# Kernel tuning notes

Measured on AMD Instinct MI355X. Metric: run time of the kernel, lower is better.

## Reference

```python
import jax, jax.numpy as jnp
import numpy as np

EPS = 1e-5  # BatchNorm eps

def _bn(x):
    # BatchNorm1d(affine=False) in training mode: per-agent, per-feature batch stats
    m = jnp.mean(x, axis=1, keepdims=True)
    v = jnp.var(x, axis=1, keepdims=True)
    return (x - m) / jnp.sqrt(v + EPS)

def _lrelu(x):
    return jax.nn.leaky_relu(x, 0.01)

def setup_inputs() -> dict:
    key = jax.random.key(0)
    ks = jax.random.split(key, 14)
    A, B, IN, OUT, H, K = 8, 32768, 128, 32, 128, 4
    D = H // K
    s = 0.05
    return {
        "states": jax.random.normal(ks[0], (A, B, IN), jnp.float32),
        "actions": jax.random.normal(ks[1], (A, B, OUT), jnp.float32),
        "enc_w": jax.random.normal(ks[2], (A, IN + OUT, H), jnp.float32) * s,
        "enc_b": jax.random.normal(ks[3], (A, H), jnp.float32) * s,
        "aenc_w": jax.random.normal(ks[4], (A, OUT, H), jnp.float32) * s,
        "aenc_b": jax.random.normal(ks[5], (A, H), jnp.float32) * s,
        "key_w": jax.random.normal(ks[6], (K, H, D), jnp.float32) * s,
        "sel_w": jax.random.normal(ks[7], (K, H, D), jnp.float32) * s,
        "val_w": jax.random.normal(ks[8], (K, H, D), jnp.float32) * s,
        "val_b": jax.random.normal(ks[9], (K, D), jnp.float32) * s,
        "c1_w": jax.random.normal(ks[10], (A, 2 * H, H), jnp.float32) * s,
        "c1_b": jax.random.normal(ks[11], (A, H), jnp.float32) * s,
        "c2_w": jax.random.normal(ks[12], (A, H, 1), jnp.float32) * s,
        "c2_b": jax.random.normal(ks[13], (A, 1), jnp.float32) * s,
    }

def reference(states, actions, enc_w, enc_b, aenc_w, aenc_b,
              key_w, sel_w, val_w, val_b, c1_w, c1_b, c2_w, c2_b):
    A, B, _ = states.shape
    # per-agent state-action encodings: [A,B,H]
    sa = _bn(jnp.concatenate([states, actions], axis=-1))
    sa_enc = _lrelu(jnp.einsum('abi,aih->abh', sa, enc_w) + enc_b[:, None, :])
    # per-agent action encodings: [A,B,H]
    a_in = _bn(actions)
    a_enc = _lrelu(jnp.einsum('abi,aih->abh', a_in, aenc_w) + aenc_b[:, None, :])
    # per-head keys/values/selectors: [K,A,B,D]
    keys = jnp.einsum('abh,khd->kabd', a_enc, key_w)
    vals = _lrelu(jnp.einsum('abh,khd->kabd', a_enc, val_w) + val_b[:, None, None, :])
    sels = jnp.einsum('abh,khd->kabd', sa_enc, sel_w)
    D = keys.shape[-1]
    # attention logits over other agents: [K,B,A_query,A_key], self excluded
    logits = jnp.einsum('kibd,kjbd->kbij', sels, keys) / jnp.sqrt(jnp.float32(D))
    self_mask = jnp.eye(A, dtype=bool)[None, None]
    probs = jax.nn.softmax(jnp.where(self_mask, -jnp.inf, logits), axis=-1)
    # attended values: [K,A,B,D] -> concat heads -> [A,B,K*D]
    other = jnp.einsum('kbij,kjbd->kibd', probs, vals)
    other_cat = jnp.transpose(other, (1, 2, 0, 3)).reshape(A, B, -1)
    # per-agent critics on [sa_enc, attended]: [A,B,1]
    critic_in = jnp.concatenate([sa_enc, other_cat], axis=-1)
    h = _lrelu(jnp.einsum('abi,aih->abh', critic_in, c1_w) + c1_b[:, None, :])
    q = jnp.einsum('abh,aho->abo', h, c2_w) + c2_b[:, None, :]
    return q
```

## Files before the change

kernel.cpp:

```cpp
#include <hip/hip_runtime.h>
#include <hip/hip_bf16.h>
#include <stdint.h>

#define A_N 8
#define B_N 32768
#define IN_N 128
#define OUT_N 32
#define SAF 160
#define H_N 128
#define D_N 32
#define KD_N 128
#define CIN_N 256
#define CHUNKS 128
#define EPSV 1e-5f
#define ENC_KP 192

typedef unsigned int u32;
typedef unsigned short u16;
typedef __attribute__((ext_vector_type(8))) short short8;
typedef __attribute__((ext_vector_type(4))) float floatx4;

__device__ __forceinline__ float bf_lo(u32 u){ return __uint_as_float(u << 16); }
__device__ __forceinline__ float bf_hi(u32 u){ return __uint_as_float(u & 0xffff0000u); }
__device__ __forceinline__ float bf2f(u16 b){ return __uint_as_float(((u32)b) << 16); }
__device__ __forceinline__ u16 f2bf(float f){
  u32 u = __float_as_uint(f);
  return (u16)((u + 0x7fffu + ((u >> 16) & 1u)) >> 16);
}
__device__ __forceinline__ float lrelu(float x){ return x > 0.f ? x : 0.01f * x; }

__global__ __launch_bounds__(256) void k_stats(
    const float* __restrict__ states, const float* __restrict__ actions,
    float* __restrict__ part)
{
  int a = blockIdx.y;
  int chunk = blockIdx.x;
  int t = threadIdx.x;
  int r0 = chunk * (B_N / CHUNKS);
  __shared__ float red[512];
  {
    int f = t & 127, half = t >> 7;
    const float* p = states + ((size_t)a * B_N + r0 + half) * IN_N + f;
    float s1 = 0.f, s2 = 0.f;
    for (int it = 0; it < 128; ++it){
      float v = p[(size_t)(2 * it) * IN_N];
      s1 += v; s2 += v * v;
    }
    red[t] = s1; red[256 + t] = s2;
    __syncthreads();
    if (t < 128){
      float a1 = red[t] + red[t + 128];
      float a2 = red[256 + t] + red[256 + t + 128];
      size_t o = (((size_t)a * CHUNKS + chunk) * SAF + t) * 2;
      part[o] = a1; part[o + 1] = a2;
    }
    __syncthreads();
  }
  {
    int f = t & 31, g = t >> 5;
    const float* p = actions + ((size_t)a * B_N + r0 + g) * OUT_N + f;
    float s1 = 0.f, s2 = 0.f;
    for (int it = 0; it < 32; ++it){
      float v = p[(size_t)(8 * it) * OUT_N];
      s1 += v; s2 += v * v;
    }
    red[t] = s1; red[256 + t] = s2;
    __syncthreads();
    if (t < 32){
      float a1 = 0.f, a2 = 0.f;
      #pragma unroll
      for (int gg = 0; gg < 8; ++gg){
        a1 += red[t + 32 * gg];
        a2 += red[256 + t + 32 * gg];
      }
      size_t o = (((size_t)a * CHUNKS + chunk) * SAF + 128 + t) * 2;
      part[o] = a1; part[o + 1] = a2;
    }
  }
}

__global__ void k_finalize(const float* __restrict__ part,
                           float* __restrict__ meanArr, float* __restrict__ istdArr)
{
  int idx = blockIdx.x * blockDim.x + threadIdx.x;
  if (idx >= A_N * SAF) return;
  int a = idx / SAF, f = idx % SAF;
  float s1 = 0.f, s2 = 0.f;
  for (int c = 0; c < CHUNKS; ++c){
    size_t o = (((size_t)a * CHUNKS + c) * SAF + f) * 2;
    s1 += part[o]; s2 += part[o + 1];
  }
  float m = s1 * (1.f / B_N);
  float v = s2 * (1.f / B_N) - m * m;
  if (v < 0.f) v = 0.f;
  meanArr[idx] = m;
  istdArr[idx] = rsqrtf(v + EPSV);
}

__device__ __forceinline__ void packpair(float w, u16* __restrict__ dh,
                                         u16* __restrict__ dl, int i){
  u16 h = f2bf(w);
  dh[i] = h;
  dl[i] = f2bf(w - bf2f(h));
}

__global__ __launch_bounds__(256) void k_pack(
    const float* __restrict__ enc_w, const float* __restrict__ aenc_w,
    const float* __restrict__ key_w, const float* __restrict__ sel_w,
    const float* __restrict__ val_w, const float* __restrict__ c1_w,
    u16* __restrict__ encH, u16* __restrict__ encL,
    u16* __restrict__ aencH, u16* __restrict__ aencL,
    u16* __restrict__ keyH, u16* __restrict__ selH, u16* __restrict__ valH,
    u16* __restrict__ c1H, u16* __restrict__ c1L)
{
  int i = blockIdx.x * 256 + threadIdx.x;
  const int S0 = A_N * H_N * ENC_KP;
  const int S1 = A_N * H_N * OUT_N;
  const int S2 = KD_N * H_N;
  const int S5 = A_N * H_N * CIN_N;
  if (i < S0){
    int a = i / (H_N * ENC_KP); int r = i % (H_N * ENC_KP);
    int n = r / ENC_KP; int k = r % ENC_KP;
    float v = (k < SAF) ? enc_w[((size_t)a * SAF + k) * H_N + n] : 0.f;
    packpair(v, encH, encL, i);
    return;
  }
  i -= S0;
  if (i < S1){
    int a = i / (H_N * OUT_N); int r = i % (H_N * OUT_N);
    int n = r / OUT_N; int k = r % OUT_N;
    packpair(aenc_w[((size_t)a * OUT_N + k) * H_N + n], aencH, aencL, i);
    return;
  }
  i -= S1;
  if (i < 3 * S2){
    int which = i / S2; int j = i % S2;
    int n = j / H_N, k = j % H_N;
    const float* w = (which == 0) ? key_w : ((which == 1) ? sel_w : val_w);
    u16* dh = (which == 0) ? keyH : ((which == 1) ? selH : valH);
    dh[j] = f2bf(w[(((size_t)(n >> 5)) * H_N + k) * D_N + (n & 31)]);
    return;
  }
  i -= 3 * S2;
  if (i < S5){
    int a = i / (H_N * CIN_N); int r = i % (H_N * CIN_N);
    int n = r / CIN_N; int k = r % CIN_N;
    packpair(c1_w[((size_t)a * CIN_N + k) * H_N + n], c1H, c1L, i);
  }
}
#define PACK_TOTAL (A_N*H_N*ENC_KP + A_N*H_N*OUT_N + 3*KD_N*H_N + A_N*H_N*CIN_N)

__global__ __launch_bounds__(256, 3) void k_enc_sel(
    const float* __restrict__ states, const float* __restrict__ actions,
    const float* __restrict__ mean, const float* __restrict__ istd,
    const u16* __restrict__ encH, const u16* __restrict__ encL,
    const float* __restrict__ enc_b,
    const u16* __restrict__ selH,
    u16* __restrict__ sa_enc, u16* __restrict__ sels)
{
  int a = blockIdx.y; int row0 = blockIdx.x * 128; int t = threadIdx.x;
  int lane = t & 63, wave = t >> 6, l16 = lane & 15, quad = lane >> 4;
  __shared__ __align__(16) u16 S[22528];
  __shared__ __align__(16) float sc[192], sh[192];
  u16* Wh = S;
  u16* Wl = S + 5120;
  u16* Xh = S + 10240;
  u16* Xl = S + 15360;
  u16* T  = S;
  u16* Ws = S + 17408;

  if (t < 192){
    float m = 0.f, s = 0.f;
    if (t < SAF){ m = mean[a * SAF + t]; s = istd[a * SAF + t]; }
    sc[t] = s; sh[t] = -m * s;
  }
  floatx4 acc[2][8];
  #pragma unroll
  for (int mt = 0; mt < 2; ++mt)
    #pragma unroll
    for (int nt = 0; nt < 8; ++nt) acc[mt][nt] = (floatx4){0.f,0.f,0.f,0.f};
  const u16* wbh = encH + (size_t)a * H_N * ENC_KP;
  const u16* wbl = encL + (size_t)a * H_N * ENC_KP;
  __syncthreads();

  for (int k0 = 0; k0 < ENC_KP; k0 += 32){
    for (int c = t; c < 512; c += 256){
      int n = c >> 2, off = (c & 3) * 8;
      *(uint4*)&Wh[n * 40 + off] = *(const uint4*)(wbh + (size_t)n * ENC_KP + k0 + off);
      *(uint4*)&Wl[n * 40 + off] = *(const uint4*)(wbl + (size_t)n * ENC_KP + k0 + off);
    }
    for (int c = t; c < 1024; c += 256){
      int r = c >> 3, kc = (c & 7) * 4, f = k0 + kc;
      size_t row = (size_t)a * B_N + row0 + r;
      float4 v = {0.f, 0.f, 0.f, 0.f};
      if (f < IN_N)     v = *(const float4*)(states + row * IN_N + f);
      else if (f < SAF) v = *(const float4*)(actions + row * OUT_N + (f - IN_N));
      float4 scv = *(const float4*)&sc[f];
      float4 shv = *(const float4*)&sh[f];
      float x0 = fmaf(v.x, scv.x, shv.x), x1 = fmaf(v.y, scv.y, shv.y);
      float x2 = fmaf(v.z, scv.z, shv.z), x3 = fmaf(v.w, scv.w, shv.w);
      u16 h0 = f2bf(x0), h1 = f2bf(x1), h2 = f2bf(x2), h3 = f2bf(x3);
      *(u32*)&Xh[r * 40 + kc]     = (u32)h0 | ((u32)h1 << 16);
      *(u32*)&Xh[r * 40 + kc + 2] = (u32)h2 | ((u32)h3 << 16);
      u16 l0 = f2bf(x0 - bf2f(h0)), l1 = f2bf(x1 - bf2f(h1));
      u16 l2 = f2bf(x2 - bf2f(h2)), l3 = f2bf(x3 - bf2f(h3));
      *(u32*)&Xl[r * 40 + kc]     = (u32)l0 | ((u32)l1 << 16);
      *(u32*)&Xl[r * 40 + kc + 2] = (u32)l2 | ((u32)l3 << 16);
    }
    __syncthreads();
    {
      short8 ah[2], al[2], bh[8], bl[8];
      #pragma unroll
      for (int mt = 0; mt < 2; ++mt){
        int rr = (wave * 32 + mt * 16 + l16) * 40 + quad * 8;
        ah[mt] = *(const short8*)&Xh[rr];
        al[mt] = *(const short8*)&Xl[rr];
      }
      #pragma unroll
      for (int nt = 0; nt < 8; ++nt){
        int rr = (nt * 16 + l16) * 40 + quad * 8;
        bh[nt] = *(const short8*)&Wh[rr];
        bl[nt] = *(const short8*)&Wl[rr];
      }
      #pragma unroll
      for (int mt = 0; mt < 2; ++mt)
        #pragma unroll
        for (int nt = 0; nt < 8; ++nt){
          acc[mt][nt] = __builtin_amdgcn_mfma_f32_16x16x32_bf16(ah[mt], bh[nt], acc[mt][nt], 0,0,0);
          acc[mt][nt] = __builtin_amdgcn_mfma_f32_16x16x32_bf16(ah[mt], bl[nt], acc[mt][nt], 0,0,0);
          acc[mt][nt] = __builtin_amdgcn_mfma_f32_16x16x32_bf16(al[mt], bh[nt], acc[mt][nt], 0,0,0);
        }
    }
    __syncthreads();
  }

  {
    float bv[8];
    #pragma unroll
    for (int nt = 0; nt < 8; ++nt) bv[nt] = enc_b[a * H_N + nt * 16 + l16];
    #pragma unroll
    for (int mt = 0; mt < 2; ++mt)
      #pragma unroll
      for (int nt = 0; nt < 8; ++nt)
        #pragma unroll
        for (int r = 0; r < 4; ++r){
          int rl = wave * 32 + mt * 16 + quad * 4 + r;
          T[rl * 136 + nt * 16 + l16] = f2bf(lrelu(acc[mt][nt][r] + bv[nt]));
        }
  }
  __syncthreads();
  for (int c = t; c < 2048; c += 256){
    int row = c >> 4, col8 = (c & 15) * 8;
    *(uint4*)(sa_enc + ((size_t)a * B_N + row0 + row) * H_N + col8) =
        *(const uint4*)&T[row * 136 + col8];
  }

  #pragma unroll
  for (int mt = 0; mt < 2; ++mt)
    #pragma unroll
    for (int nt = 0; nt < 8; ++nt) acc[mt][nt] = (floatx4){0.f,0.f,0.f,0.f};
  for (int k0 = 0; k0 < H_N; k0 += 32){
    for (int c = t; c < 512; c += 256){
      int n = c >> 2, off = (c & 3) * 8;
      *(uint4*)&Ws[n * 40 + off] = *(const uint4*)(selH + (size_t)n * H_N + k0 + off);
    }
    __syncthreads();
    {
      short8 ah[2], bh[8];
      #pragma unroll
      for (int mt = 0; mt < 2; ++mt)
        ah[mt] = *(const short8*)&T[(wave * 32 + mt * 16 + l16) * 136 + k0 + quad * 8];
      #pragma unroll
      for (int nt = 0; nt < 8; ++nt)
        bh[nt] = *(const short8*)&Ws[(nt * 16 + l16) * 40 + quad * 8];
      #pragma unroll
      for (int mt = 0; mt < 2; ++mt)
        #pragma unroll
        for (int nt = 0; nt < 8; ++nt)
          acc[mt][nt] = __builtin_amdgcn_mfma_f32_16x16x32_bf16(ah[mt], bh[nt], acc[mt][nt], 0,0,0);
    }
    __syncthreads();
  }
  #pragma unroll
  for (int mt = 0; mt < 2; ++mt)
    #pragma unroll
    for (int nt = 0; nt < 8; ++nt)
      #pragma unroll
      for (int r = 0; r < 4; ++r){
        int rl = wave * 32 + mt * 16 + quad * 4 + r;
        T[rl * 136 + nt * 16 + l16] = f2bf(acc[mt][nt][r]);
      }
  __syncthreads();
  for (int c = t; c < 2048; c += 256){
    int row = c >> 4, col8 = (c & 15) * 8;
    *(uint4*)(sels + ((size_t)a * B_N + row0 + row) * H_N + col8) =
        *(const uint4*)&T[row * 136 + col8];
  }
}

__global__ __launch_bounds__(256, 2) void k_aenc_kv(
    const float* __restrict__ actions,
    const float* __restrict__ mean, const float* __restrict__ istd,
    const u16* __restrict__ aencH, const u16* __restrict__ aencL,
    const float* __restrict__ aenc_b,
    const u16* __restrict__ keyH, const u16* __restrict__ valH,
    const float* __restrict__ val_b,
    u16* __restrict__ keys, u16* __restrict__ vals)
{
  int a = blockIdx.y; int row0 = blockIdx.x * 128; int t = threadIdx.x;
  int lane = t & 63, wave = t >> 6, l16 = lane & 15, quad = lane >> 4;
  __shared__ __align__(16) u16 S[35840];
  __shared__ __align__(16) float sc[32], sh[32];
  u16* T  = S;
  u16* WK = S + 17408;
  u16* WV = S + 26624;
  u16* T2 = S + 17408;

  if (t < 32){
    float m = mean[a * SAF + 128 + t], s = istd[a * SAF + 128 + t];
    sc[t] = s; sh[t] = -m * s;
  }
  floatx4 accK[2][8], accV[2][8];
  #pragma unroll
  for (int mt = 0; mt < 2; ++mt)
    #pragma unroll
    for (int nt = 0; nt < 8; ++nt){
      accK[mt][nt] = (floatx4){0.f,0.f,0.f,0.f};
      accV[mt][nt] = (floatx4){0.f,0.f,0.f,0.f};
    }
  __syncthreads();

  {
    u16* Wh1 = S;  u16* Wl1 = S + 5120;
    u16* Xh = S + 10240; u16* Xl = S + 15360;
    const u16* wbh = aencH + (size_t)a * H_N * OUT_N;
    const u16* wbl = aencL + (size_t)a * H_N * OUT_N;
    for (int c = t; c < 512; c += 256){
      int n = c >> 2, off = (c & 3) * 8;
      *(uint4*)&Wh1[n * 40 + off] = *(const uint4*)(wbh + (size_t)n * OUT_N + off);
      *(uint4*)&Wl1[n * 40 + off] = *(const uint4*)(wbl + (size_t)n * OUT_N + off);
    }
    for (int c = t; c < 1024; c += 256){
      int r = c >> 3, kc = (c & 7) * 4;
      size_t row = (size_t)a * B_N + row0 + r;
      float4 v = *(const float4*)(actions + row * OUT_N + kc);
      float4 scv = *(const float4*)&sc[kc];
      float4 shv = *(const float4*)&sh[kc];
      float x0 = fmaf(v.x, scv.x, shv.x), x1 = fmaf(v.y, scv.y, shv.y);
      float x2 = fmaf(v.z, scv.z, shv.z), x3 = fmaf(v.w, scv.w, shv.w);
      u16 h0 = f2bf(x0), h1 = f2bf(x1), h2 = f2bf(x2), h3 = f2bf(x3);
      *(u32*)&Xh[r * 40 + kc]     = (u32)h0 | ((u32)h1 << 16);
      *(u32*)&Xh[r * 40 + kc + 2] = (u32)h2 | ((u32)h3 << 16);
      u16 l0 = f2bf(x0 - bf2f(h0)), l1 = f2bf(x1 - bf2f(h1));
      u16 l2 = f2bf(x2 - bf2f(h2)), l3 = f2bf(x3 - bf2f(h3));
      *(u32*)&Xl[r * 40 + kc]     = (u32)l0 | ((u32)l1 << 16);
      *(u32*)&Xl[r * 40 + kc + 2] = (u32)l2 | ((u32)l3 << 16);
    }
    __syncthreads();
    short8 ah[2], al[2], bh[8], bl[8];
    #pragma unroll
    for (int mt = 0; mt < 2; ++mt){
      int rr = (wave * 32 + mt * 16 + l16) * 40 + quad * 8;
      ah[mt] = *(const short8*)&Xh[rr];
      al[mt] = *(const short8*)&Xl[rr];
    }
    #pragma unroll
    for (int nt = 0; nt < 8; ++nt){
      int rr = (nt * 16 + l16) * 40 + quad * 8;
      bh[nt] = *(const short8*)&Wh1[rr];
      bl[nt] = *(const short8*)&Wl1[rr];
    }
    #pragma unroll
    for (int mt = 0; mt < 2; ++mt)
      #pragma unroll
      for (int nt = 0; nt < 8; ++nt){
        accK[mt][nt] = __builtin_amdgcn_mfma_f32_16x16x32_bf16(ah[mt], bh[nt], accK[mt][nt], 0,0,0);
        accK[mt][nt] = __builtin_amdgcn_mfma_f32_16x16x32_bf16(ah[mt], bl[nt], accK[mt][nt], 0,0,0);
        accK[mt][nt] = __builtin_amdgcn_mfma_f32_16x16x32_bf16(al[mt], bh[nt], accK[mt][nt], 0,0,0);
      }
    __syncthreads();
  }
  {
    float bv[8];
    #pragma unroll
    for (int nt = 0; nt < 8; ++nt) bv[nt] = aenc_b[a * H_N + nt * 16 + l16];
    #pragma unroll
    for (int mt = 0; mt < 2; ++mt)
      #pragma unroll
      for (int nt = 0; nt < 8; ++nt){
        #pragma unroll
        for (int r = 0; r < 4; ++r){
          int rl = wave * 32 + mt * 16 + quad * 4 + r;
          T[rl * 136 + nt * 16 + l16] = f2bf(lrelu(accK[mt][nt][r] + bv[nt]));
        }
        accK[mt][nt] = (floatx4){0.f,0.f,0.f,0.f};
      }
  }

  for (int k0 = 0; k0 < H_N; k0 += 64){
    __syncthreads();
    for (int c = t; c < 1024; c += 256){
      int n = c >> 3, off = (c & 7) * 8;
      *(uint4*)&WK[n * 72 + off] = *(const uint4*)(keyH + (size_t)n * H_N + k0 + off);
      *(uint4*)&WV[n * 72 + off] = *(const uint4*)(valH + (size_t)n * H_N + k0 + off);
    }
    __syncthreads();
    #pragma unroll
    for (int ks = 0; ks < 64; ks += 32){
      short8 ah[2], bk[8], bv[8];
      #pragma unroll
      for (int mt = 0; mt < 2; ++mt)
        ah[mt] = *(const short8*)&T[(wave * 32 + mt * 16 + l16) * 136 + k0 + ks + quad * 8];
      #pragma unroll
      for (int nt = 0; nt < 8; ++nt){
        int rr = (nt * 16 + l16) * 72 + ks + quad * 8;
        bk[nt] = *(const short8*)&WK[rr];
        bv[nt] = *(const short8*)&WV[rr];
      }
      #pragma unroll
      for (int mt = 0; mt < 2; ++mt)
        #pragma unroll
        for (int nt = 0; nt < 8; ++nt){
          accK[mt][nt] = __builtin_amdgcn_mfma_f32_16x16x32_bf16(ah[mt], bk[nt], accK[mt][nt], 0,0,0);
          accV[mt][nt] = __builtin_amdgcn_mfma_f32_16x16x32_bf16(ah[mt], bv[nt], accV[mt][nt], 0,0,0);
        }
    }
  }
  __syncthreads();
  {
    float bv[8];
    #pragma unroll
    for (int nt = 0; nt < 8; ++nt) bv[nt] = val_b[nt * 16 + l16];
    #pragma unroll
    for (int mt = 0; mt < 2; ++mt)
      #pragma unroll
      for (int nt = 0; nt < 8; ++nt)
        #pragma unroll
        for (int r = 0; r < 4; ++r){
          int rl = wave * 32 + mt * 16 + quad * 4 + r;
          T[rl * 136 + nt * 16 + l16]  = f2bf(lrelu(accV[mt][nt][r] + bv[nt]));
          T2[rl * 136 + nt * 16 + l16] = f2bf(accK[mt][nt][r]);
        }
  }
  __syncthreads();
  for (int c = t; c < 2048; c += 256){
    int row = c >> 4, col8 = (c & 15) * 8;
    *(uint4*)(vals + ((size_t)a * B_N + row0 + row) * H_N + col8) =
        *(const uint4*)&T[row * 136 + col8];
    *(uint4*)(keys + ((size_t)a * B_N + row0 + row) * H_N + col8) =
        *(const uint4*)&T2[row * 136 + col8];
  }
}

__global__ __launch_bounds__(256) void k_attn(
    const u16* __restrict__ sels, const u16* __restrict__ keys,
    const u16* __restrict__ vals, u16* __restrict__ other)
{
  int b0 = blockIdx.x * 8;
  int t = threadIdx.x;
  __shared__ __align__(16) u16 sS[8192], sK[8192], sV[8192];
  u32* dS = (u32*)sS; u32* dK = (u32*)sK; u32* dV = (u32*)sV;
  #pragma unroll
  for (int a = 0; a < 8; ++a){
    size_t go = ((size_t)a * B_N + b0) * KD_N;
    const u32* gs = (const u32*)(sels + go);
    const u32* gk = (const u32*)(keys + go);
    const u32* gv = (const u32*)(vals + go);
    dS[a * 512 + t] = gs[t]; dS[a * 512 + 256 + t] = gs[256 + t];
    dK[a * 512 + t] = gk[t]; dK[a * 512 + 256 + t] = gk[256 + t];
    dV[a * 512 + t] = gv[t]; dV[a * 512 + 256 + t] = gv[256 + t];
  }
  __syncthreads();
  int i = t & 7, p = t >> 3;
  int k = p & 3, bl = p >> 2;
  int base_i = (i * 8 + bl) * 128 + k * 32;
  float si[32];
  {
    const u32* S32 = (const u32*)&sS[base_i];
    #pragma unroll
    for (int d2 = 0; d2 < 16; ++d2){
      u32 u = S32[d2];
      si[2 * d2] = bf_lo(u); si[2 * d2 + 1] = bf_hi(u);
    }
  }
  float lg[8];
  #pragma unroll
  for (int j = 0; j < 8; ++j){
    const u32* K32 = (const u32*)&sK[(j * 8 + bl) * 128 + k * 32];
    float acc = 0.f;
    #pragma unroll
    for (int d2 = 0; d2 < 16; ++d2){
      u32 u = K32[d2];
      acc = fmaf(si[2 * d2], bf_lo(u), acc);
      acc = fmaf(si[2 * d2 + 1], bf_hi(u), acc);
    }
    lg[j] = acc * 0.17677669529663689f;
  }
  float mx = -3.0e38f;
  #pragma unroll
  for (int j = 0; j < 8; ++j) if (j != i) mx = fmaxf(mx, lg[j]);
  float pe[8], se = 0.f;
  #pragma unroll
  for (int j = 0; j < 8; ++j){
    pe[j] = (j == i) ? 0.f : __expf(lg[j] - mx);
    se += pe[j];
  }
  float inv = 1.f / se;
  #pragma unroll
  for (int j = 0; j < 8; ++j) pe[j] *= inv;
  __align__(16) u16 ob[32];
  #pragma unroll
  for (int d2 = 0; d2 < 16; ++d2){
    float acc0 = 0.f, acc1 = 0.f;
    #pragma unroll
    for (int j = 0; j < 8; ++j){
      u32 u = *(const u32*)&sV[(j * 8 + bl) * 128 + k * 32 + 2 * d2];
      acc0 = fmaf(pe[j], bf_lo(u), acc0);
      acc1 = fmaf(pe[j], bf_hi(u), acc1);
    }
    ob[2 * d2] = f2bf(acc0); ob[2 * d2 + 1] = f2bf(acc1);
  }
  uint4* dst = (uint4*)(other + ((size_t)i * B_N + (b0 + bl)) * KD_N + k * 32);
  const uint4* s4 = (const uint4*)ob;
  #pragma unroll
  for (int c = 0; c < 4; ++c) dst[c] = s4[c];
}

__global__ __launch_bounds__(256, 3) void k_critic(
    const u16* __restrict__ sa_enc, const u16* __restrict__ other,
    const u16* __restrict__ c1H, const u16* __restrict__ c1L,
    const float* __restrict__ c1_b,
    const float* __restrict__ c2w, const float* __restrict__ c2b,
    float* __restrict__ qout)
{
  int a = blockIdx.y; int row0 = blockIdx.x * 128; int t = threadIdx.x;
  int lane = t & 63, wave = t >> 6, l16 = lane & 15, quad = lane >> 4;
  __shared__ __align__(16) u16 Xs[5120];
  __shared__ __align__(16) u16 Wh[5120];
  __shared__ __align__(16) u16 Wl[5120];
  floatx4 acc[2][8];
  #pragma unroll
  for (int mt = 0; mt < 2; ++mt)
    #pragma unroll
    for (int nt = 0; nt < 8; ++nt) acc[mt][nt] = (floatx4){0.f,0.f,0.f,0.f};
  const u16* wbh = c1H + (size_t)a * H_N * CIN_N;
  const u16* wbl = c1L + (size_t)a * H_N * CIN_N;

  for (int k0 = 0; k0 < CIN_N; k0 += 32){
    for (int c = t; c < 512; c += 256){
      int n = c >> 2, off = (c & 3) * 8;
      *(uint4*)&Wh[n * 40 + off] = *(const uint4*)(wbh + (size_t)n * CIN_N + k0 + off);
      *(uint4*)&Wl[n * 40 + off] = *(const uint4*)(wbl + (size_t)n * CIN_N + k0 + off);
    }
    for (int c = t; c < 512; c += 256){
      int r = c >> 2, off = (c & 3) * 8;
      int fo = k0 + off;
      const u16* src = sa_enc;
      if (fo >= H_N){ src = other; fo -= H_N; }
      *(uint4*)&Xs[r * 40 + off] =
          *(const uint4*)(src + ((size_t)a * B_N + row0 + r) * H_N + fo);
    }
    __syncthreads();
    {
      short8 ah[2], bh[8], bl[8];
      #pragma unroll
      for (int mt = 0; mt < 2; ++mt)
        ah[mt] = *(const short8*)&Xs[(wave * 32 + mt * 16 + l16) * 40 + quad * 8];
      #pragma unroll
      for (int nt = 0; nt < 8; ++nt){
        int rr = (nt * 16 + l16) * 40 + quad * 8;
        bh[nt] = *(const short8*)&Wh[rr];
        bl[nt] = *(const short8*)&Wl[rr];
      }
      #pragma unroll
      for (int mt = 0; mt < 2; ++mt)
        #pragma unroll
        for (int nt = 0; nt < 8; ++nt){
          acc[mt][nt] = __builtin_amdgcn_mfma_f32_16x16x32_bf16(ah[mt], bh[nt], acc[mt][nt], 0,0,0);
          acc[mt][nt] = __builtin_amdgcn_mfma_f32_16x16x32_bf16(ah[mt], bl[nt], acc[mt][nt], 0,0,0);
        }
    }
    __syncthreads();
  }

  float c2r[8], bv[8];
  #pragma unroll
  for (int nt = 0; nt < 8; ++nt){
    c2r[nt] = c2w[a * H_N + nt * 16 + l16];
    bv[nt]  = c1_b[a * H_N + nt * 16 + l16];
  }
  #pragma unroll
  for (int mt = 0; mt < 2; ++mt){
    #pragma unroll
    for (int r = 0; r < 4; ++r){
      float s = 0.f;
      #pragma unroll
      for (int nt = 0; nt < 8; ++nt){
        float h = lrelu(acc[mt][nt][r] + bv[nt]);
        s = fmaf(h, c2r[nt], s);
      }
      s += __shfl_xor(s, 1);
      s += __shfl_xor(s, 2);
      s += __shfl_xor(s, 4);
      s += __shfl_xor(s, 8);
      if (l16 == 0){
        int row = row0 + wave * 32 + mt * 16 + quad * 4 + r;
        qout[(size_t)a * B_N + row] = s + c2b[a];
      }
    }
  }
}

extern "C" void kernel_launch(void* const* d_in, const int* in_sizes, int n_in,
                              void* d_out, int out_size, void* d_ws, size_t ws_size,
                              hipStream_t stream)
{
  const float* states  = (const float*)d_in[0];
  const float* actions = (const float*)d_in[1];
  const float* enc_w   = (const float*)d_in[2];
  const float* enc_b   = (const float*)d_in[3];
  const float* aenc_w  = (const float*)d_in[4];
  const float* aenc_b  = (const float*)d_in[5];
  const float* key_w   = (const float*)d_in[6];
  const float* sel_w   = (const float*)d_in[7];
  const float* val_w   = (const float*)d_in[8];
  const float* val_b   = (const float*)d_in[9];
  const float* c1_w    = (const float*)d_in[10];
  const float* c1_b    = (const float*)d_in[11];
  const float* c2_w    = (const float*)d_in[12];
  const float* c2_b    = (const float*)d_in[13];
  float* q = (float*)d_out;

  char* ws = (char*)d_ws;
  u16* encH  = (u16*)(ws + 0);
  u16* encL  = (u16*)(ws + 393216);
  u16* aencH = (u16*)(ws + 786432);
  u16* aencL = (u16*)(ws + 851968);
  u16* keyH  = (u16*)(ws + 917504);
  u16* selH  = (u16*)(ws + 950272);
  u16* valH  = (u16*)(ws + 983040);
  float* part    = (float*)ws;
  float* meanArr = (float*)(ws + 1310720);
  float* istdArr = (float*)(ws + 1315840);
  u16* c1H = (u16*)(ws + 1320960);
  u16* c1L = (u16*)(ws + 1845248);
  const size_t ibase = 4194304;
  const size_t BUF = (size_t)A_N * B_N * 128 * 2;
  u16* sa_enc = (u16*)(ws + ibase);
  u16* sels   = (u16*)(ws + ibase + BUF);
  u16* keys   = (u16*)(ws + ibase + 2 * BUF);
  u16* vals   = (u16*)(ws + ibase + 3 * BUF);

  k_stats<<<dim3(CHUNKS, A_N), 256, 0, stream>>>(states, actions, part);
  k_finalize<<<(A_N * SAF + 255) / 256, 256, 0, stream>>>(part, meanArr, istdArr);
  k_pack<<<(PACK_TOTAL + 255) / 256, 256, 0, stream>>>(
      enc_w, aenc_w, key_w, sel_w, val_w, c1_w,
      encH, encL, aencH, aencL, keyH, selH, valH, c1H, c1L);

  dim3 g(B_N / 128, A_N);
  k_enc_sel<<<g, 256, 0, stream>>>(states, actions, meanArr, istdArr,
                                   encH, encL, enc_b, selH, sa_enc, sels);
  k_aenc_kv<<<g, 256, 0, stream>>>(actions, meanArr, istdArr,
                                   aencH, aencL, aenc_b, keyH, valH, val_b,
                                   keys, vals);
  k_attn<<<B_N / 8, 256, 0, stream>>>(sels, keys, vals, keys);
  k_critic<<<g, 256, 0, stream>>>(sa_enc, keys, c1H, c1L, c1_b, c2_w, c2_b, q);
}
```

Measured before the change: 536.4 us.

## Pre-tile packed weights and stream tiles into LDS with global_load_lds

Repacks all bf16 weight matrices into contiguous 32-wide K tiles so each tile can be copied straight into shared memory with direct global-to-LDS loads. This bypasses VGPRs, drops the zero-padded K=192 enc layout, and also uses global_load_lds for the critic's activation tiles. LDS row strides shrink from 40/72 to 32 without padding, which may bring back bank conflicts on the MFMA operand reads. The attention kernel's staging loads are widened to 16-byte vectors.

```diff
diff --git a/kernel.cpp b/kernel.cpp
--- a/kernel.cpp
+++ b/kernel.cpp
@@ -13,12 +13,17 @@
 #define CIN_N 256
 #define CHUNKS 128
 #define EPSV 1e-5f
-#define ENC_KP 192
 
 typedef unsigned int u32;
 typedef unsigned short u16;
 typedef __attribute__((ext_vector_type(8))) short short8;
 typedef __attribute__((ext_vector_type(4))) float floatx4;
+
+typedef __attribute__((address_space(1))) void gvoid;
+typedef __attribute__((address_space(3))) void lvoid;
+__device__ __forceinline__ void glds16(const void* g, void* l){
+  __builtin_amdgcn_global_load_lds((gvoid*)g, (lvoid*)l, 16, 0, 0);
+}
 
 __device__ __forceinline__ float bf_lo(u32 u){ return __uint_as_float(u << 16); }
 __device__ __forceinline__ float bf_hi(u32 u){ return __uint_as_float(u & 0xffff0000u); }
@@ -114,41 +119,46 @@
     u16* __restrict__ c1H, u16* __restrict__ c1L)
 {
   int i = blockIdx.x * 256 + threadIdx.x;
-  const int S0 = A_N * H_N * ENC_KP;
+  const int S0 = A_N * H_N * SAF;
   const int S1 = A_N * H_N * OUT_N;
   const int S2 = KD_N * H_N;
   const int S5 = A_N * H_N * CIN_N;
   if (i < S0){
-    int a = i / (H_N * ENC_KP); int r = i % (H_N * ENC_KP);
-    int n = r / ENC_KP; int k = r % ENC_KP;
-    float v = (k < SAF) ? enc_w[((size_t)a * SAF + k) * H_N + n] : 0.f;
-    packpair(v, encH, encL, i);
+    int a = i / (H_N * SAF); int r = i % (H_N * SAF);
+    int tile = r >> 12; int rr = r & 4095;
+    int n = rr >> 5; int kk = rr & 31;
+    int kg = tile * 32 + kk;
+    packpair(enc_w[((size_t)a * SAF + kg) * H_N + n], encH, encL, i);
     return;
   }
   i -= S0;
   if (i < S1){
-    int a = i / (H_N * OUT_N); int r = i % (H_N * OUT_N);
-    int n = r / OUT_N; int k = r % OUT_N;
+    int a = i >> 12; int rr = i & 4095;
+    int n = rr >> 5; int k = rr & 31;
     packpair(aenc_w[((size_t)a * OUT_N + k) * H_N + n], aencH, aencL, i);
     return;
   }
   i -= S1;
   if (i < 3 * S2){
     int which = i / S2; int j = i % S2;
-    int n = j / H_N, k = j % H_N;
+    int tile = j >> 12; int rr = j & 4095;
+    int n = rr >> 5; int kk = rr & 31;
+    int kg = tile * 32 + kk;
     const float* w = (which == 0) ? key_w : ((which == 1) ? sel_w : val_w);
     u16* dh = (which == 0) ? keyH : ((which == 1) ? selH : valH);
-    dh[j] = f2bf(w[(((size_t)(n >> 5)) * H_N + k) * D_N + (n & 31)]);
+    dh[j] = f2bf(w[(((size_t)(n >> 5)) * H_N + kg) * D_N + (n & 31)]);
     return;
   }
   i -= 3 * S2;
   if (i < S5){
-    int a = i / (H_N * CIN_N); int r = i % (H_N * CIN_N);
-    int n = r / CIN_N; int k = r % CIN_N;
-    packpair(c1_w[((size_t)a * CIN_N + k) * H_N + n], c1H, c1L, i);
-  }
-}
-#define PACK_TOTAL (A_N*H_N*ENC_KP + A_N*H_N*OUT_N + 3*KD_N*H_N + A_N*H_N*CIN_N)
+    int a = i >> 15; int r = i & 32767;
+    int tile = r >> 12; int rr = r & 4095;
+    int n = rr >> 5; int kk = rr & 31;
+    int kg = tile * 32 + kk;
+    packpair(c1_w[((size_t)a * CIN_N + kg) * H_N + n], c1H, c1L, i);
+  }
+}
+#define PACK_TOTAL (A_N*H_N*SAF + A_N*H_N*OUT_N + 3*KD_N*H_N + A_N*H_N*CIN_N)
 
 __global__ __launch_bounds__(256, 3) void k_enc_sel(
     const float* __restrict__ states, const float* __restrict__ actions,
@@ -160,18 +170,17 @@
 {
   int a = blockIdx.y; int row0 = blockIdx.x * 128; int t = threadIdx.x;
   int lane = t & 63, wave = t >> 6, l16 = lane & 15, quad = lane >> 4;
-  __shared__ __align__(16) u16 S[22528];
-  __shared__ __align__(16) float sc[192], sh[192];
+  __shared__ __align__(16) u16 S[25600];
+  __shared__ __align__(16) float sc[160], sh[160];
   u16* Wh = S;
-  u16* Wl = S + 5120;
-  u16* Xh = S + 10240;
-  u16* Xl = S + 15360;
+  u16* Wl = S + 4096;
+  u16* Xh = S + 8192;
+  u16* Xl = S + 13312;
   u16* T  = S;
   u16* Ws = S + 17408;
 
-  if (t < 192){
-    float m = 0.f, s = 0.f;
-    if (t < SAF){ m = mean[a * SAF + t]; s = istd[a * SAF + t]; }
+  if (t < SAF){
+    float m = mean[a * SAF + t], s = istd[a * SAF + t];
     sc[t] = s; sh[t] = -m * s;
   }
   floatx4 acc[2][8];
@@ -179,33 +188,35 @@
   for (int mt = 0; mt < 2; ++mt)
     #pragma unroll
     for (int nt = 0; nt < 8; ++nt) acc[mt][nt] = (floatx4){0.f,0.f,0.f,0.f};
-  const u16* wbh = encH + (size_t)a * H_N * ENC_KP;
-  const u16* wbl = encL + (size_t)a * H_N * ENC_KP;
+  const u16* ebh = encH + (size_t)a * (H_N * SAF);
+  const u16* ebl = encL + (size_t)a * (H_N * SAF);
   __syncthreads();
 
-  for (int k0 = 0; k0 < ENC_KP; k0 += 32){
+  for (int k0 = 0; k0 < SAF; k0 += 32){
+    const u16* th = ebh + (k0 >> 5) * 4096;
+    const u16* tl = ebl + (k0 >> 5) * 4096;
+    #pragma unroll
     for (int c = t; c < 512; c += 256){
-      int n = c >> 2, off = (c & 3) * 8;
-      *(uint4*)&Wh[n * 40 + off] = *(const uint4*)(wbh + (size_t)n * ENC_KP + k0 + off);
-      *(uint4*)&Wl[n * 40 + off] = *(const uint4*)(wbl + (size_t)n * ENC_KP + k0 + off);
+      glds16(th + c * 8, Wh + c * 8);
+      glds16(tl + c * 8, Wl + c * 8);
     }
     for (int c = t; c < 1024; c += 256){
       int r = c >> 3, kc = (c & 7) * 4, f = k0 + kc;
       size_t row = (size_t)a * B_N + row0 + r;
-      float4 v = {0.f, 0.f, 0.f, 0.f};
-      if (f < IN_N)     v = *(const float4*)(states + row * IN_N + f);
-      else if (f < SAF) v = *(const float4*)(actions + row * OUT_N + (f - IN_N));
+      float4 v;
+      if (f < IN_N) v = *(const float4*)(states + row * IN_N + f);
+      else          v = *(const float4*)(actions + row * OUT_N + (f - IN_N));
       float4 scv = *(const float4*)&sc[f];
       float4 shv = *(const float4*)&sh[f];
       float x0 = fmaf(v.x, scv.x, shv.x), x1 = fmaf(v.y, scv.y, shv.y);
       float x2 = fmaf(v.z, scv.z, shv.z), x3 = fmaf(v.w, scv.w, shv.w);
       u16 h0 = f2bf(x0), h1 = f2bf(x1), h2 = f2bf(x2), h3 = f2bf(x3);
-      *(u32*)&Xh[r * 40 + kc]     = (u32)h0 | ((u32)h1 << 16);
-      *(u32*)&Xh[r * 40 + kc + 2] = (u32)h2 | ((u32)h3 << 16);
+      uint2 hv; hv.x = (u32)h0 | ((u32)h1 << 16); hv.y = (u32)h2 | ((u32)h3 << 16);
+      *(uint2*)&Xh[r * 40 + kc] = hv;
       u16 l0 = f2bf(x0 - bf2f(h0)), l1 = f2bf(x1 - bf2f(h1));
       u16 l2 = f2bf(x2 - bf2f(h2)), l3 = f2bf(x3 - bf2f(h3));
-      *(u32*)&Xl[r * 40 + kc]     = (u32)l0 | ((u32)l1 << 16);
-      *(u32*)&Xl[r * 40 + kc + 2] = (u32)l2 | ((u32)l3 << 16);
+      uint2 lv; lv.x = (u32)l0 | ((u32)l1 << 16); lv.y = (u32)l2 | ((u32)l3 << 16);
+      *(uint2*)&Xl[r * 40 + kc] = lv;
     }
     __syncthreads();
     {
@@ -218,7 +229,7 @@
       }
       #pragma unroll
       for (int nt = 0; nt < 8; ++nt){
-        int rr = (nt * 16 + l16) * 40 + quad * 8;
+        int rr = (nt * 16 + l16) * 32 + quad * 8;
         bh[nt] = *(const short8*)&Wh[rr];
         bl[nt] = *(const short8*)&Wl[rr];
       }
@@ -259,20 +270,20 @@
   for (int mt = 0; mt < 2; ++mt)
     #pragma unroll
     for (int nt = 0; nt < 8; ++nt) acc[mt][nt] = (floatx4){0.f,0.f,0.f,0.f};
-  for (int k0 = 0; k0 < H_N; k0 += 32){
-    for (int c = t; c < 512; c += 256){
-      int n = c >> 2, off = (c & 3) * 8;
-      *(uint4*)&Ws[n * 40 + off] = *(const uint4*)(selH + (size_t)n * H_N + k0 + off);
-    }
-    __syncthreads();
-    {
+  for (int k0 = 0; k0 < H_N; k0 += 64){
+    #pragma unroll
+    for (int c = t; c < 1024; c += 256)
+      glds16(selH + (k0 >> 5) * 4096 + c * 8, Ws + c * 8);
+    __syncthreads();
+    #pragma unroll
+    for (int ks = 0; ks < 64; ks += 32){
       short8 ah[2], bh[8];
       #pragma unroll
       for (int mt = 0; mt < 2; ++mt)
-        ah[mt] = *(const short8*)&T[(wave * 32 + mt * 16 + l16) * 136 + k0 + quad * 8];
+        ah[mt] = *(const short8*)&T[(wave * 32 + mt * 16 + l16) * 136 + k0 + ks + quad * 8];
       #pragma unroll
       for (int nt = 0; nt < 8; ++nt)
-        bh[nt] = *(const short8*)&Ws[(nt * 16 + l16) * 40 + quad * 8];
+        bh[nt] = *(const short8*)&Ws[((ks >> 5) << 12) + (nt * 16 + l16) * 32 + quad * 8];
       #pragma unroll
       for (int mt = 0; mt < 2; ++mt)
         #pragma unroll
@@ -309,11 +320,11 @@
 {
   int a = blockIdx.y; int row0 = blockIdx.x * 128; int t = threadIdx.x;
   int lane = t & 63, wave = t >> 6, l16 = lane & 15, quad = lane >> 4;
-  __shared__ __align__(16) u16 S[35840];
+  __shared__ __align__(16) u16 S[34816];
   __shared__ __align__(16) float sc[32], sh[32];
   u16* T  = S;
   u16* WK = S + 17408;
-  u16* WV = S + 26624;
+  u16* WV = S + 25600;
   u16* T2 = S + 17408;
 
   if (t < 32){
@@ -331,14 +342,14 @@
   __syncthreads();
 
   {
-    u16* Wh1 = S;  u16* Wl1 = S + 5120;
-    u16* Xh = S + 10240; u16* Xl = S + 15360;
-    const u16* wbh = aencH + (size_t)a * H_N * OUT_N;
-    const u16* wbl = aencL + (size_t)a * H_N * OUT_N;
+    u16* Wh1 = S;  u16* Wl1 = S + 4096;
+    u16* Xh = S + 8192; u16* Xl = S + 13312;
+    const u16* abh = aencH + (size_t)a * 4096;
+    const u16* abl = aencL + (size_t)a * 4096;
+    #pragma unroll
     for (int c = t; c < 512; c += 256){
-      int n = c >> 2, off = (c & 3) * 8;
-      *(uint4*)&Wh1[n * 40 + off] = *(const uint4*)(wbh + (size_t)n * OUT_N + off);
-      *(uint4*)&Wl1[n * 40 + off] = *(const uint4*)(wbl + (size_t)n * OUT_N + off);
+      glds16(abh + c * 8, Wh1 + c * 8);
+      glds16(abl + c * 8, Wl1 + c * 8);
     }
     for (int c = t; c < 1024; c += 256){
       int r = c >> 3, kc = (c & 7) * 4;
@@ -349,12 +360,12 @@
       float x0 = fmaf(v.x, scv.x, shv.x), x1 = fmaf(v.y, scv.y, shv.y);
       float x2 = fmaf(v.z, scv.z, shv.z), x3 = fmaf(v.w, scv.w, shv.w);
       u16 h0 = f2bf(x0), h1 = f2bf(x1), h2 = f2bf(x2), h3 = f2bf(x3);
-      *(u32*)&Xh[r * 40 + kc]     = (u32)h0 | ((u32)h1 << 16);
-      *(u32*)&Xh[r * 40 + kc + 2] = (u32)h2 | ((u32)h3 << 16);
+      uint2 hv; hv.x = (u32)h0 | ((u32)h1 << 16); hv.y = (u32)h2 | ((u32)h3 << 16);
+      *(uint2*)&Xh[r * 40 + kc] = hv;
       u16 l0 = f2bf(x0 - bf2f(h0)), l1 = f2bf(x1 - bf2f(h1));
       u16 l2 = f2bf(x2 - bf2f(h2)), l3 = f2bf(x3 - bf2f(h3));
-      *(u32*)&Xl[r * 40 + kc]     = (u32)l0 | ((u32)l1 << 16);
-      *(u32*)&Xl[r * 40 + kc + 2] = (u32)l2 | ((u32)l3 << 16);
+      uint2 lv; lv.x = (u32)l0 | ((u32)l1 << 16); lv.y = (u32)l2 | ((u32)l3 << 16);
+      *(uint2*)&Xl[r * 40 + kc] = lv;
     }
     __syncthreads();
     short8 ah[2], al[2], bh[8], bl[8];
@@ -366,7 +377,7 @@
     }
     #pragma unroll
     for (int nt = 0; nt < 8; ++nt){
-      int rr = (nt * 16 + l16) * 40 + quad * 8;
+      int rr = (nt * 16 + l16) * 32 + quad * 8;
       bh[nt] = *(const short8*)&Wh1[rr];
       bl[nt] = *(const short8*)&Wl1[rr];
     }
@@ -399,10 +410,10 @@
 
   for (int k0 = 0; k0 < H_N; k0 += 64){
     __syncthreads();
+    #pragma unroll
     for (int c = t; c < 1024; c += 256){
-      int n = c >> 3, off = (c & 7) * 8;
-      *(uint4*)&WK[n * 72 + off] = *(const uint4*)(keyH + (size_t)n * H_N + k0 + off);
-      *(uint4*)&WV[n * 72 + off] = *(const uint4*)(valH + (size_t)n * H_N + k0 + off);
+      glds16(keyH + (k0 >> 5) * 4096 + c * 8, WK + c * 8);
+      glds16(valH + (k0 >> 5) * 4096 + c * 8, WV + c * 8);
     }
     __syncthreads();
     #pragma unroll
@@ -413,7 +424,7 @@
         ah[mt] = *(const short8*)&T[(wave * 32 + mt * 16 + l16) * 136 + k0 + ks + quad * 8];
       #pragma unroll
       for (int nt = 0; nt < 8; ++nt){
-        int rr = (nt * 16 + l16) * 72 + ks + quad * 8;
+        int rr = ((ks >> 5) << 12) + (nt * 16 + l16) * 32 + quad * 8;
         bk[nt] = *(const short8*)&WK[rr];
         bv[nt] = *(const short8*)&WV[rr];
       }
@@ -459,16 +470,16 @@
   int b0 = blockIdx.x * 8;
   int t = threadIdx.x;
   __shared__ __align__(16) u16 sS[8192], sK[8192], sV[8192];
-  u32* dS = (u32*)sS; u32* dK = (u32*)sK; u32* dV = (u32*)sV;
-  #pragma unroll
-  for (int a = 0; a < 8; ++a){
-    size_t go = ((size_t)a * B_N + b0) * KD_N;
-    const u32* gs = (const u32*)(sels + go);
-    const u32* gk = (const u32*)(keys + go);
-    const u32* gv = (const u32*)(vals + go);
-    dS[a * 512 + t] = gs[t]; dS[a * 512 + 256 + t] = gs[256 + t];
-    dK[a * 512 + t] = gk[t]; dK[a * 512 + 256 + t] = gk[256 + t];
-    dV[a * 512 + t] = gv[t]; dV[a * 512 + 256 + t] = gv[256 + t];
+  {
+    uint4* dS4 = (uint4*)sS; uint4* dK4 = (uint4*)sK; uint4* dV4 = (uint4*)sV;
+    #pragma unroll
+    for (int c = t; c < 1024; c += 256){
+      int aa = c >> 7, o = c & 127;
+      size_t go = ((size_t)aa * B_N + b0) * KD_N;
+      dS4[c] = *((const uint4*)(sels + go) + o);
+      dK4[c] = *((const uint4*)(keys + go) + o);
+      dV4[c] = *((const uint4*)(vals + go) + o);
+    }
   }
   __syncthreads();
   int i = t & 7, p = t >> 3;
@@ -535,40 +546,43 @@
 {
   int a = blockIdx.y; int row0 = blockIdx.x * 128; int t = threadIdx.x;
   int lane = t & 63, wave = t >> 6, l16 = lane & 15, quad = lane >> 4;
-  __shared__ __align__(16) u16 Xs[5120];
-  __shared__ __align__(16) u16 Wh[5120];
-  __shared__ __align__(16) u16 Wl[5120];
+  __shared__ __align__(16) u16 Xs[4096];
+  __shared__ __align__(16) u16 Wh[4096];
+  __shared__ __align__(16) u16 Wl[4096];
   floatx4 acc[2][8];
   #pragma unroll
   for (int mt = 0; mt < 2; ++mt)
     #pragma unroll
     for (int nt = 0; nt < 8; ++nt) acc[mt][nt] = (floatx4){0.f,0.f,0.f,0.f};
-  const u16* wbh = c1H + (size_t)a * H_N * CIN_N;
-  const u16* wbl = c1L + (size_t)a * H_N * CIN_N;
+  const u16* wbh = c1H + (size_t)a * (H_N * CIN_N);
+  const u16* wbl = c1L + (size_t)a * (H_N * CIN_N);
 
   for (int k0 = 0; k0 < CIN_N; k0 += 32){
+    const u16* th = wbh + (k0 >> 5) * 4096;
+    const u16* tl = wbl + (k0 >> 5) * 4096;
+    #pragma unroll
     for (int c = t; c < 512; c += 256){
-      int n = c >> 2, off = (c & 3) * 8;
-      *(uint4*)&Wh[n * 40 + off] = *(const uint4*)(wbh + (size_t)n * CIN_N + k0 + off);
-      *(uint4*)&Wl[n * 40 + off] = *(const uint4*)(wbl + (size_t)n * CIN_N + k0 + off);
-    }
-    for (int c = t; c < 512; c += 256){
-      int r = c >> 2, off = (c & 3) * 8;
-      int fo = k0 + off;
-      const u16* src = sa_enc;
-      if (fo >= H_N){ src = other; fo -= H_N; }
-      *(uint4*)&Xs[r * 40 + off] =
-          *(const uint4*)(src + ((size_t)a * B_N + row0 + r) * H_N + fo);
+      glds16(th + c * 8, Wh + c * 8);
+      glds16(tl + c * 8, Wl + c * 8);
+    }
+    {
+      const u16* src = (k0 < H_N) ? sa_enc : other;
+      int kb = (k0 < H_N) ? k0 : k0 - H_N;
+      #pragma unroll
+      for (int c = t; c < 512; c += 256){
+        int r = c >> 2, off = (c & 3) * 8;
+        glds16(src + ((size_t)a * B_N + row0 + r) * H_N + kb + off, Xs + c * 8);
+      }
     }
     __syncthreads();
     {
       short8 ah[2], bh[8], bl[8];
       #pragma unroll
       for (int mt = 0; mt < 2; ++mt)
-        ah[mt] = *(const short8*)&Xs[(wave * 32 + mt * 16 + l16) * 40 + quad * 8];
+        ah[mt] = *(const short8*)&Xs[(wave * 32 + mt * 16 + l16) * 32 + quad * 8];
       #pragma unroll
       for (int nt = 0; nt < 8; ++nt){
-        int rr = (nt * 16 + l16) * 40 + quad * 8;
+        int rr = (nt * 16 + l16) * 32 + quad * 8;
         bh[nt] = *(const short8*)&Wh[rr];
         bl[nt] = *(const short8*)&Wl[rr];
       }
@@ -633,12 +647,12 @@
 
   char* ws = (char*)d_ws;
   u16* encH  = (u16*)(ws + 0);
-  u16* encL  = (u16*)(ws + 393216);
-  u16* aencH = (u16*)(ws + 786432);
-  u16* aencL = (u16*)(ws + 851968);
-  u16* keyH  = (u16*)(ws + 917504);
-  u16* selH  = (u16*)(ws + 950272);
-  u16* valH  = (u16*)(ws + 983040);
+  u16* encL  = (u16*)(ws + 327680);
+  u16* aencH = (u16*)(ws + 655360);
+  u16* aencL = (u16*)(ws + 720896);
+  u16* keyH  = (u16*)(ws + 786432);
+  u16* selH  = (u16*)(ws + 819200);
+  u16* valH  = (u16*)(ws + 851968);
   float* part    = (float*)ws;
   float* meanArr = (float*)(ws + 1310720);
   float* istdArr = (float*)(ws + 1315840);
```

Result: faster. 509.8 us (-5.0%).
